# Kernel tuning notes

Measured on AMD Instinct MI355X. Metric: run time of the kernel, lower is better.

The kernel has to match this reference:

```python
import jax, jax.numpy as jnp
from jax import lax
import numpy as np

DECAY = 0.5   # LIF membrane leak factor
VTH = 1.0     # firing threshold


def _conv(x, w, stride, pad):
    # x: [B,C,H,W], w: [O,I,kh,kw]
    return lax.conv_general_dilated(
        x, w, (stride, stride), [(pad, pad), (pad, pad)],
        dimension_numbers=('NCHW', 'OIHW', 'NCHW'))


def _convT(x, w, b, stride=2, pad=1):
    # torch ConvTranspose2d(in,out,k,stride,pad): w is [Cin,Cout,k,k]
    k = w.shape[-1]
    wf = jnp.flip(w, (-2, -1)).transpose(1, 0, 2, 3)  # -> [Cout,Cin,k,k]
    y = lax.conv_general_dilated(
        x, wf, (1, 1), [(k - 1 - pad, k - 1 - pad)] * 2,
        lhs_dilation=(stride, stride),
        dimension_numbers=('NCHW', 'OIHW', 'NCHW'))
    return y + b[None, :, None, None]


def setup_inputs() -> dict:
    key = jax.random.key(0)
    ks = jax.random.split(key, 8)
    T, B = 16, 32
    x_seq = (jax.random.uniform(ks[0], (T, B, 1, 100, 368)) < 0.1).astype(jnp.float32)

    def p(k, shape, fan_in):
        return jax.random.normal(k, shape, jnp.float32) * (1.0 / np.sqrt(fan_in))

    return {
        'x_seq': x_seq,
        'w1': p(ks[1], (16, 1, 5, 5), 25),
        'w2': p(ks[2], (32, 16, 3, 3), 16 * 9),
        'wd': p(ks[3], (64, 32, 3, 3), 32 * 9),
        'bd': jnp.zeros((64,), jnp.float32),
        'wt1': p(ks[4], (64, 32, 4, 4), 64 * 16),
        'bt1': jnp.zeros((32,), jnp.float32),
        'wt2': p(ks[5], (32, 2, 4, 4), 32 * 16),
        'bt2': jnp.zeros((2,), jnp.float32),
        'actual_batch_size': 32,
    }


def reference(x_seq, w1, w2, wd, bd, wt1, bt1, wt2, bt2, actual_batch_size):
    B = x_seq.shape[1]
    dt = x_seq.dtype
    mem1 = jnp.zeros((B, 16, 50, 184), dt)
    mem2 = jnp.zeros((B, 32, 25, 92), dt)

    def step(carry, x):
        m1, m2 = carry
        # spiking conv layer 1: leaky integrate, fire, hard reset
        m1 = m1 * DECAY + _conv(x, w1, 2, 2)
        s1 = (m1 >= VTH).astype(dt)
        m1 = m1 * (1.0 - s1)
        # spiking conv layer 2 (return_dense -> membrane kept for decoder)
        m2 = m2 * DECAY + _conv(s1, w2, 2, 1)
        s2 = (m2 >= VTH).astype(dt)
        m2 = m2 * (1.0 - s2)
        return (m1, m2), None

    (mem1, mem2), _ = lax.scan(step, (mem1, mem2), x_seq)

    # dense CNN decoder on final membrane state
    h = jax.nn.relu(_conv(mem2, wd, 1, 1) + bd[None, :, None, None])   # [B,64,25,92]
    h = jax.nn.relu(_convT(h, wt1, bt1))                               # [B,32,50,184]
    out = jax.nn.softplus(_convT(h, wt2, bt2))                         # [B,2,100,368]
    inv_tau_c_pred = out[:, 0:1]
    alpha_pred = out[:, 1:2]
    return inv_tau_c_pred, alpha_pred
```

## Files before the change

### kernel.cpp

```cpp
#include <hip/hip_runtime.h>
#include <hip/hip_bf16.h>
#include <cstddef>


#define T_STEPS 16
#define NB 32
#define H0 100
#define W0 368
#define C1 16
#define H1 50
#define W1 184
#define C2 32
#define H2 25
#define W2 92
#define CD 64
#define WPR 6
#define SITES2 2300
#define SITES1 9200
#define NPOS1 (NB * H1 * W1)

using f32x16 = __attribute__((ext_vector_type(16))) float;
using f32x4  = __attribute__((ext_vector_type(4))) float;
using s16x8  = __attribute__((ext_vector_type(8))) short;

__device__ inline unsigned short f2bf(float f) {
    union { float f; unsigned int u; } v; v.f = f;
    unsigned int r = v.u + 0x7fffu + ((v.u >> 16) & 1u);
    return (unsigned short)(r >> 16);
}
__device__ inline float bf2f(unsigned short u) {
    union { unsigned int u; float f; } v; v.u = ((unsigned int)u) << 16;
    return v.f;
}
__device__ inline unsigned int pk2(float a, float b) {
    return (unsigned int)f2bf(a) | ((unsigned int)f2bf(b) << 16);
}
__device__ inline s16x8 ld8(const void* p) { return *reinterpret_cast<const s16x8*>(p); }

__global__ __launch_bounds__(256) void k_pack(const float* __restrict__ x,
                                              unsigned long long* __restrict__ xb) {
    int widx = blockIdx.x * 4 + (threadIdx.x >> 6);
    int lane = threadIdx.x & 63;
    int rowid = widx / WPR;
    int wcol  = widx - rowid * WPR;
    int col = (wcol << 6) + lane;
    const float* rp = x + (size_t)rowid * W0;
    float v = 0.f;
    if (col < W0) v = rp[col];
    unsigned long long m = __ballot(v != 0.f);
    if (lane == 0) xb[widx] = m;
}

__global__ __launch_bounds__(256) void k_mask(const unsigned long long* __restrict__ xb,
                                              unsigned int* __restrict__ bm) {
    int gid = blockIdx.x * blockDim.x + threadIdx.x;
    int t = gid / NPOS1;
    int site = gid - t * NPOS1;
    int x1 = site % W1;
    int tq = site / W1;
    int y1 = tq % H1;
    int b  = tq / H1;
    const int iy0 = 2 * y1 - 2;
    const int ix0 = 2 * x1 - 2;
    const int wi = ix0 >> 6;
    const int sh = ix0 & 63;
    const unsigned long long* xp = xb + ((size_t)(t * NB + b) * H0) * WPR;
    unsigned int bits25 = 0;
#pragma unroll
    for (int ky = 0; ky < 5; ++ky) {
        int iy = iy0 + ky;
        if (iy < 0 || iy >= H0) continue;
        const unsigned long long* row = xp + (size_t)iy * WPR;
        unsigned long long a = (wi >= 0) ? row[wi] : 0ull;
        unsigned long long bw = (wi + 1 < WPR) ? row[wi + 1] : 0ull;
        unsigned long long chunk = a >> sh;
        if (sh) chunk |= (bw << (64 - sh));
        bits25 |= ((unsigned int)chunk & 31u) << (5 * ky);
    }
    bm[gid] = bits25;
}

__global__ __launch_bounds__(256) void k_snn1(const unsigned int* __restrict__ bm,
                                              const unsigned short* __restrict__ w1b3,
                                              unsigned char* __restrict__ s1b) {
    __shared__ uint4 lut[256];
    {
        int m = (int)threadIdx.x;
        unsigned int wv[4];
#pragma unroll
        for (int h = 0; h < 4; ++h) {
            unsigned int lo = (m >> (2 * h)) & 1u, hb = (m >> (2 * h + 1)) & 1u;
            wv[h] = (lo ? 0x3F80u : 0u) | (hb ? 0x3F800000u : 0u);
        }
        lut[m] = make_uint4(wv[0], wv[1], wv[2], wv[3]);
    }
    __syncthreads();

    int wave = threadIdx.x >> 6;
    int lane = threadIdx.x & 63;
    int col = lane & 15;
    int hi  = lane >> 4;
    int base = (blockIdx.x * 4 + wave) * 64;

    s16x8 af0 = ld8((const char*)w1b3 + (size_t)((0 * 16 + col) * 32 + hi * 8) * 2);
    s16x8 af1 = ld8((const char*)w1b3 + (size_t)((1 * 16 + col) * 32 + hi * 8) * 2);
    s16x8 af2 = ld8((const char*)w1b3 + (size_t)((2 * 16 + col) * 32 + hi * 8) * 2);

    f32x4 acc0 = {}, acc1 = {}, acc2 = {}, acc3 = {};

    unsigned int cm0, cm1, cm2, cm3;
    {
        const unsigned int* bp = bm + base;
        cm0 = bp[col]; cm1 = bp[16 + col]; cm2 = bp[32 + col]; cm3 = bp[48 + col];
    }

    for (int t = 0; t < T_STEPS; ++t) {
        unsigned int nm0 = 0, nm1 = 0, nm2 = 0, nm3 = 0;
        if (t < T_STEPS - 1) {
            const unsigned int* bp = bm + (size_t)(t + 1) * NPOS1 + base;
            nm0 = bp[col]; nm1 = bp[16 + col]; nm2 = bp[32 + col]; nm3 = bp[48 + col];
        }
#pragma unroll
        for (int e = 0; e < 4; ++e) {
            acc0[e] *= 0.5f; acc1[e] *= 0.5f; acc2[e] *= 0.5f; acc3[e] *= 0.5f;
        }
#pragma unroll
        for (int g = 0; g < 4; ++g) {
            unsigned int sb = (g == 0) ? cm0 : (g == 1) ? cm1 : (g == 2) ? cm2 : cm3;
            unsigned int byte = (sb >> (hi * 8)) & 0xFFu;
            s16x8 bf = *reinterpret_cast<const s16x8*>(&lut[byte]);
            f32x4& ac = (g == 0) ? acc0 : (g == 1) ? acc1 : (g == 2) ? acc2 : acc3;
            ac = __builtin_amdgcn_mfma_f32_16x16x32_bf16(af0, bf, ac, 0, 0, 0);
            ac = __builtin_amdgcn_mfma_f32_16x16x32_bf16(af1, bf, ac, 0, 0, 0);
            ac = __builtin_amdgcn_mfma_f32_16x16x32_bf16(af2, bf, ac, 0, 0, 0);
        }
#pragma unroll
        for (int g = 0; g < 4; ++g) {
            f32x4& ac = (g == 0) ? acc0 : (g == 1) ? acc1 : (g == 2) ? acc2 : acc3;
            unsigned int nib = 0;
#pragma unroll
            for (int e = 0; e < 4; ++e) {
                float v = ac[e];
                bool s = (v >= 1.0f);
                if (s) nib |= (1u << e);
                ac[e] = s ? 0.f : v;
            }
            unsigned int mk = nib << ((hi & 1) * 4);
            mk |= __shfl_xor(mk, 16, 64);
            if (hi == 0)
                s1b[(size_t)(t * 2 + 0) * NPOS1 + base + g * 16 + col] = (unsigned char)mk;
            else if (hi == 2)
                s1b[(size_t)(t * 2 + 1) * NPOS1 + base + g * 16 + col] = (unsigned char)mk;
        }
        cm0 = nm0; cm1 = nm1; cm2 = nm2; cm3 = nm3;
    }
}

__global__ __launch_bounds__(256) void k_snn2(const unsigned char* __restrict__ s1b,
                                              const unsigned short* __restrict__ w2b3,
                                              unsigned short* __restrict__ mem2bf) {
    __shared__ uint4 lut[256];
    {
        int m = (int)threadIdx.x;
        unsigned int wv[4];
#pragma unroll
        for (int h = 0; h < 4; ++h) {
            unsigned int lo = (m >> (2 * h)) & 1u, hb = (m >> (2 * h + 1)) & 1u;
            wv[h] = (lo ? 0x3F80u : 0u) | (hb ? 0x3F800000u : 0u);
        }
        lut[m] = make_uint4(wv[0], wv[1], wv[2], wv[3]);
    }
    __syncthreads();

    int wave = threadIdx.x >> 6;
    int lane = threadIdx.x & 63;
    int col = lane & 31, hi = lane >> 5;
    int gsite = (blockIdx.x * 4 + wave) * 32 + col;
    int b = gsite / SITES2;
    int rest = gsite % SITES2;
    int y2 = rest / W2, x2 = rest % W2;

    int toff[9]; bool tval[9];
#pragma unroll
    for (int ky = 0; ky < 3; ++ky)
#pragma unroll
        for (int kx = 0; kx < 3; ++kx) {
            int iy = 2 * y2 + ky - 1, ix = 2 * x2 + kx - 1;
            tval[ky * 3 + kx] = iy >= 0 && iy < H1 && ix >= 0 && ix < W1;
            toff[ky * 3 + kx] = iy * W1 + ix;
        }

    const char* ab = (const char*)w2b3;
    s16x8 a0[9], a1[9], a2[9];
#pragma unroll
    for (int s = 0; s < 9; ++s) {
        int ko = (s * 16 + hi * 8) * 2;
        a0[s] = ld8(ab + (col * 144) * 2 + ko);
        a1[s] = ld8(ab + ((32 + col) * 144) * 2 + ko);
        a2[s] = ld8(ab + ((64 + col) * 144) * 2 + ko);
    }

    f32x16 acc = {};

    unsigned int msk[9];
    {
        const unsigned char* spk = s1b + (size_t)hi * NPOS1 + (size_t)b * (H1 * W1);
#pragma unroll
        for (int i = 0; i < 9; ++i)
            msk[i] = tval[i] ? (unsigned int)spk[toff[i]] : 0u;
    }

    for (int t = 0; t < T_STEPS; ++t) {
        unsigned int nmsk[9];
#pragma unroll
        for (int i = 0; i < 9; ++i) nmsk[i] = 0u;
        if (t < T_STEPS - 1) {
            const unsigned char* spk = s1b + (size_t)((t + 1) * 2 + hi) * NPOS1 + (size_t)b * (H1 * W1);
#pragma unroll
            for (int i = 0; i < 9; ++i)
                nmsk[i] = tval[i] ? (unsigned int)spk[toff[i]] : 0u;
        }

#pragma unroll
        for (int e = 0; e < 16; ++e) acc[e] *= 0.5f;

#pragma unroll
        for (int s = 0; s < 9; ++s) {
            s16x8 bf = *reinterpret_cast<const s16x8*>(&lut[msk[s]]);
            acc = __builtin_amdgcn_mfma_f32_32x32x16_bf16(a0[s], bf, acc, 0, 0, 0);
            acc = __builtin_amdgcn_mfma_f32_32x32x16_bf16(a1[s], bf, acc, 0, 0, 0);
            acc = __builtin_amdgcn_mfma_f32_32x32x16_bf16(a2[s], bf, acc, 0, 0, 0);
        }
#pragma unroll
        for (int e = 0; e < 16; ++e) {
            float v = acc[e];
            acc[e] = (v >= 1.0f) ? 0.f : v;
        }
#pragma unroll
        for (int i = 0; i < 9; ++i) msk[i] = nmsk[i];
    }

    char* obase = (char*)(mem2bf + (size_t)gsite * C2);
#pragma unroll
    for (int q = 0; q < 4; ++q) {
        int co = 8 * q + 4 * hi;
        uint2 u;
        u.x = pk2(acc[4 * q + 0], acc[4 * q + 1]);
        u.y = pk2(acc[4 * q + 2], acc[4 * q + 3]);
        *(uint2*)(obase + co * 2) = u;
    }
}

__global__ __launch_bounds__(256) void k_repackb(const float* __restrict__ wd,
                                                 const float* __restrict__ wt1,
                                                 const float* __restrict__ wt2,
                                                 const float* __restrict__ w2,
                                                 const float* __restrict__ w1,
                                                 unsigned short* __restrict__ wdb,
                                                 unsigned short* __restrict__ wt1b,
                                                 float* __restrict__ wt2k,
                                                 unsigned short* __restrict__ w2b3,
                                                 unsigned short* __restrict__ w1b3) {
    int gid = blockIdx.x * blockDim.x + threadIdx.x;
    if (gid < 64 * 288) {
        int co = gid / 288, k = gid % 288;
        int tap = k >> 5, ci = k & 31;
        wdb[gid] = f2bf(wd[((size_t)co * C2 + ci) * 9 + tap]);
    } else if (gid < 64 * 288 + 4 * 32 * 256) {
        int j = gid - 64 * 288;
        int par = j >> 13, co = (j >> 8) & 31, k = j & 255;
        int tap = k >> 6, ci = k & 63;
        int ty = tap >> 1, tx = tap & 1;
        int ry = par >> 1, rx = par & 1;
        int ky = ry ? (ty ? 0 : 2) : (ty ? 3 : 1);
        int kx = rx ? (tx ? 0 : 2) : (tx ? 3 : 1);
        wt1b[j] = f2bf(wt1[(((size_t)ci * 32 + co) * 4 + ky) * 4 + kx]);
    } else if (gid < 64 * 288 + 4 * 32 * 256 + 1024) {
        int j = gid - (64 * 288 + 4 * 32 * 256);
        int par = j >> 8, tap = (j >> 6) & 3, ci = (j >> 1) & 31, co = j & 1;
        int ty = tap >> 1, tx = tap & 1;
        int ry = par >> 1, rx = par & 1;
        int ky = ry ? (ty ? 0 : 2) : (ty ? 3 : 1);
        int kx = rx ? (tx ? 0 : 2) : (tx ? 3 : 1);
        wt2k[j] = wt2[(((size_t)ci * 2 + co) * 4 + ky) * 4 + kx];
    } else if (gid < 64 * 288 + 4 * 32 * 256 + 1024 + 3 * 32 * 144) {
        int j = gid - (64 * 288 + 4 * 32 * 256 + 1024);
        int p = j / 4608, rem = j % 4608;
        int co = rem / 144, k = rem % 144;
        int tap = k / 16, ci = k % 16;
        float w = w2[((size_t)co * C1 + ci) * 9 + tap];
        unsigned short b0 = f2bf(w);
        float r1 = w - bf2f(b0);
        unsigned short b1 = f2bf(r1);
        float r2 = r1 - bf2f(b1);
        unsigned short b2 = f2bf(r2);
        w2b3[j] = (p == 0) ? b0 : (p == 1) ? b1 : b2;
    } else if (gid < 64 * 288 + 4 * 32 * 256 + 1024 + 3 * 32 * 144 + 3 * 16 * 32) {
        int j = gid - (64 * 288 + 4 * 32 * 256 + 1024 + 3 * 32 * 144);
        int p = j / 512, rem = j % 512;
        int co = rem / 32, k = rem % 32;
        float w = (k < 25) ? w1[co * 25 + k] : 0.f;
        unsigned short b0 = f2bf(w);
        float r1 = w - bf2f(b0);
        unsigned short b1 = f2bf(r1);
        float r2 = r1 - bf2f(b1);
        unsigned short b2 = f2bf(r2);
        w1b3[j] = (p == 0) ? b0 : (p == 1) ? b1 : b2;
    }
}

__global__ __launch_bounds__(256) void k_convd(const unsigned short* __restrict__ mem2bf,
                                               const unsigned short* __restrict__ wdb,
                                               const float* __restrict__ bd,
                                               unsigned short* __restrict__ h1bf) {
    int wave = threadIdx.x >> 6;
    int lane = threadIdx.x & 63;
    int col = lane & 31, hi = lane >> 5;
    int cog = blockIdx.y;
    int b = blockIdx.z;
    int n0 = (blockIdx.x * 4 + wave) * 32;
    int site = n0 + col;
    bool sval = site < SITES2;
    int sc = sval ? site : 0;
    int yy = sc / W2, xx = sc % W2;

    const char* ibase = (const char*)(mem2bf + (size_t)b * SITES2 * C2);
    int toff[9];
    bool tval[9];
#pragma unroll
    for (int ky = 0; ky < 3; ++ky)
#pragma unroll
        for (int kx = 0; kx < 3; ++kx) {
            int iy = yy + ky - 1, ix = xx + kx - 1;
            bool v = sval && iy >= 0 && iy < H2 && ix >= 0 && ix < W2;
            tval[ky * 3 + kx] = v;
            toff[ky * 3 + kx] = (iy * W2 + ix) * (C2 * 2);
        }

    const s16x8 zero = {0, 0, 0, 0, 0, 0, 0, 0};
    s16x8 bfr[18];
#pragma unroll
    for (int s = 0; s < 18; ++s) {
        int tap = s >> 1;
        int boff = (s & 1) * 32 + hi * 16;
        bfr[s] = tval[tap] ? ld8(ibase + toff[tap] + boff) : zero;
    }
    const char* abase = (const char*)wdb + (size_t)(cog * 32 + col) * 576 + hi * 16;
    s16x8 ar[18];
#pragma unroll
    for (int s = 0; s < 18; ++s)
        ar[s] = ld8(abase + s * 32);

    f32x16 acc = {};
#pragma unroll
    for (int s = 0; s < 18; ++s)
        acc = __builtin_amdgcn_mfma_f32_32x32x16_bf16(ar[s], bfr[s], acc, 0, 0, 0);

    if (!sval) return;
    char* obase = (char*)(h1bf + ((size_t)b * SITES2 + site) * CD);
#pragma unroll
    for (int q = 0; q < 4; ++q) {
        int co = cog * 32 + 8 * q + 4 * hi;
        float v0 = fmaxf(acc[4 * q + 0] + bd[co + 0], 0.f);
        float v1 = fmaxf(acc[4 * q + 1] + bd[co + 1], 0.f);
        float v2 = fmaxf(acc[4 * q + 2] + bd[co + 2], 0.f);
        float v3 = fmaxf(acc[4 * q + 3] + bd[co + 3], 0.f);
        uint2 u; u.x = pk2(v0, v1); u.y = pk2(v2, v3);
        *(uint2*)(obase + co * 2) = u;
    }
}

__global__ __launch_bounds__(256) void k_convt1(const unsigned short* __restrict__ h1bf,
                                                const unsigned short* __restrict__ wt1b,
                                                const float* __restrict__ bt1,
                                                unsigned short* __restrict__ h2bf) {
    int par = threadIdx.x >> 6;
    int lane = threadIdx.x & 63;
    int col = lane & 31, hi = lane >> 5;
    int ry = par >> 1, rx = par & 1;
    int b = blockIdx.z;
    int bx = blockIdx.x;
    int tile = (bx & 7) * 9 + (bx >> 3);
    int n0 = tile * 32;

    const char* ibase = (const char*)(h1bf + (size_t)b * SITES2 * CD);
    int site = n0 + col;
    bool sv = site < SITES2;
    int sc = sv ? site : 0;
    int m = sc / W2, n = sc % W2;
    int iy1 = m + (ry ? 1 : -1);
    int ix1 = n + (rx ? 1 : -1);
    bool y1v = iy1 >= 0 && iy1 < H2;
    bool x1v = ix1 >= 0 && ix1 < W2;
    int toff[4]; bool tval[4];
#pragma unroll
    for (int t = 0; t < 4; ++t) {
        int ty = t >> 1, tx = t & 1;
        int iy = ty ? iy1 : m;
        int ix = tx ? ix1 : n;
        tval[t] = sv && (ty ? y1v : true) && (tx ? x1v : true);
        toff[t] = (iy * W2 + ix) * (CD * 2);
    }

    const s16x8 zero = {0, 0, 0, 0, 0, 0, 0, 0};
    s16x8 bfr[16];
#pragma unroll
    for (int s = 0; s < 16; ++s) {
        int tap = s >> 2;
        int boff = (s & 3) * 32 + hi * 16;
        bfr[s] = tval[tap] ? ld8(ibase + toff[tap] + boff) : zero;
    }
    const char* abase = (const char*)(wt1b + (size_t)par * 32 * 256) + (size_t)col * 512 + hi * 16;
    s16x8 ar[16];
#pragma unroll
    for (int s = 0; s < 16; ++s)
        ar[s] = ld8(abase + s * 32);

    f32x16 acc = {};
#pragma unroll
    for (int s = 0; s < 16; ++s)
        acc = __builtin_amdgcn_mfma_f32_32x32x16_bf16(ar[s], bfr[s], acc, 0, 0, 0);

    if (!sv) return;
    int oy = 2 * m + ry, ox = 2 * n + rx;
    char* obase = (char*)(h2bf + ((size_t)b * SITES1 + (size_t)oy * W1 + ox) * C2);
#pragma unroll
    for (int q = 0; q < 4; ++q) {
        int co = 8 * q + 4 * hi;
        float v0 = fmaxf(acc[4 * q + 0] + bt1[co + 0], 0.f);
        float v1 = fmaxf(acc[4 * q + 1] + bt1[co + 1], 0.f);
        float v2 = fmaxf(acc[4 * q + 2] + bt1[co + 2], 0.f);
        float v3 = fmaxf(acc[4 * q + 3] + bt1[co + 3], 0.f);
        uint2 u; u.x = pk2(v0, v1); u.y = pk2(v2, v3);
        *(uint2*)(obase + co * 2) = u;
    }
}

__global__ __launch_bounds__(256) void k_convt2(const unsigned short* __restrict__ h2bf,
                                                const float* __restrict__ wt2k,
                                                const float* __restrict__ bt2,
                                                float* __restrict__ out) {
    int i = blockIdx.x * blockDim.x + threadIdx.x;
    if (i >= SITES1) return;
    int par = blockIdx.y;
    int ry = par >> 1, rx = par & 1;
    int b = blockIdx.z;
    int m = i / W1, n = i % W1;
    int iy1 = m + (ry ? 1 : -1);
    int ix1 = n + (rx ? 1 : -1);
    bool y1v = iy1 >= 0 && iy1 < H1;
    bool x1v = ix1 >= 0 && ix1 < W1;

    float a0 = bt2[0], a1 = bt2[1];
    const unsigned short* ib = h2bf + (size_t)b * SITES1 * C2;
#pragma unroll
    for (int t = 0; t < 4; ++t) {
        int ty = t >> 1, tx = t & 1;
        if ((ty && !y1v) || (tx && !x1v)) continue;
        int iy = ty ? iy1 : m;
        int ix = tx ? ix1 : n;
        const unsigned short* p = ib + ((size_t)iy * W1 + ix) * C2;
        const float* w = wt2k + ((size_t)par * 4 + t) * 64;
#pragma unroll
        for (int g = 0; g < 4; ++g) {
            s16x8 v8 = ld8(p + g * 8);
#pragma unroll
            for (int e = 0; e < 8; ++e) {
                float v = bf2f((unsigned short)v8[e]);
                int ci = g * 8 + e;
                a0 += v * w[2 * ci];
                a1 += v * w[2 * ci + 1];
            }
        }
    }
    int oy = 2 * m + ry, ox = 2 * n + rx;
    size_t base_o = (size_t)b * (H0 * W0) + (size_t)oy * W0 + ox;
    out[base_o] = fmaxf(a0, 0.f) + log1pf(expf(-fabsf(a0)));
    out[(size_t)NB * H0 * W0 + base_o] = fmaxf(a1, 0.f) + log1pf(expf(-fabsf(a1)));
}

extern "C" void kernel_launch(void* const* d_in, const int* in_sizes, int n_in,
                              void* d_out, int out_size, void* d_ws, size_t ws_size,
                              hipStream_t stream) {
    const float* x   = (const float*)d_in[0];
    const float* w1  = (const float*)d_in[1];
    const float* w2  = (const float*)d_in[2];
    const float* wd  = (const float*)d_in[3];
    const float* bd  = (const float*)d_in[4];
    const float* wt1 = (const float*)d_in[5];
    const float* bt1 = (const float*)d_in[6];
    const float* wt2 = (const float*)d_in[7];
    const float* bt2 = (const float*)d_in[8];
    float* out = (float*)d_out;

    char* ws = (char*)d_ws;
    unsigned char* s1b     = (unsigned char*)(ws);
    unsigned short* mem2bf = (unsigned short*)(ws + 9420800);
    unsigned short* h1bf   = (unsigned short*)(ws + 14131200);
    unsigned short* h2bf   = (unsigned short*)(ws + 23552000);
    unsigned long long* xb = (unsigned long long*)(ws + 42393600);
    unsigned short* wdb    = (unsigned short*)(ws + 44851200);
    unsigned short* wt1b   = (unsigned short*)(ws + 44888064);
    float* wt2k            = (float*)(ws + 44953600);
    unsigned short* w2b3   = (unsigned short*)(ws + 44957696);
    unsigned short* w1b3   = (unsigned short*)(ws + 44985344);
    unsigned int* bm       = (unsigned int*)(ws + 44988416);

    {
        int n = 64 * 288 + 4 * 32 * 256 + 1024 + 3 * 32 * 144 + 3 * 16 * 32;
        k_repackb<<<(n + 255) / 256, 256, 0, stream>>>(wd, wt1, wt2, w2, w1,
                                                       wdb, wt1b, wt2k, w2b3, w1b3);
    }
    {
        k_pack<<<76800, 256, 0, stream>>>(x, xb);
    }
    {
        k_mask<<<18400, 256, 0, stream>>>(xb, bm);
    }
    {
        k_snn1<<<1150, 256, 0, stream>>>(bm, w1b3, s1b);
    }
    {
        k_snn2<<<575, 256, 0, stream>>>(s1b, w2b3, mem2bf);
    }
    {
        dim3 g(18, 2, NB);
        k_convd<<<g, 256, 0, stream>>>(mem2bf, wdb, bd, h1bf);
    }
    {
        dim3 g(72, 1, NB);
        k_convt1<<<g, 256, 0, stream>>>(h1bf, wt1b, bt1, h2bf);
    }
    {
        dim3 g(36, 4, NB);
        k_convt2<<<g, 256, 0, stream>>>(h2bf, wt2k, bt2, out);
    }
}
```

Baseline: 208.6 us.

## Parallelize SNN layer-2 across timesteps with per-wave conv and LDS recurrence

```diff
diff --git a/kernel.cpp b/kernel.cpp
--- a/kernel.cpp
+++ b/kernel.cpp
@@ -156,11 +156,12 @@
     }
 }
 
-__global__ __launch_bounds__(256) void k_snn2(const unsigned char* __restrict__ s1b,
-                                              const unsigned short* __restrict__ w2b3,
-                                              unsigned short* __restrict__ mem2bf) {
+__global__ __launch_bounds__(512, 4) void k_snn2(const unsigned char* __restrict__ s1b,
+                                                 const unsigned short* __restrict__ w2b3,
+                                                 unsigned short* __restrict__ mem2bf) {
     __shared__ uint4 lut[256];
-    {
+    __shared__ float ct[8][1088];
+    if (threadIdx.x < 256) {
         int m = (int)threadIdx.x;
         unsigned int wv[4];
 #pragma unroll
@@ -175,7 +176,7 @@
     int wave = threadIdx.x >> 6;
     int lane = threadIdx.x & 63;
     int col = lane & 31, hi = lane >> 5;
-    int gsite = (blockIdx.x * 4 + wave) * 32 + col;
+    int gsite = blockIdx.x * 32 + col;
     int b = gsite / SITES2;
     int rest = gsite % SITES2;
     int y2 = rest / W2, x2 = rest % W2;
@@ -190,65 +191,59 @@
             toff[ky * 3 + kx] = iy * W1 + ix;
         }
 
+    unsigned int mskA[9], mskB[9];
+    {
+        const unsigned char* spkA = s1b + (size_t)(wave * 2 + hi) * NPOS1 + (size_t)b * (H1 * W1);
+        const unsigned char* spkB = s1b + (size_t)((wave + 8) * 2 + hi) * NPOS1 + (size_t)b * (H1 * W1);
+#pragma unroll
+        for (int i = 0; i < 9; ++i) {
+            mskA[i] = tval[i] ? (unsigned int)spkA[toff[i]] : 0u;
+            mskB[i] = tval[i] ? (unsigned int)spkB[toff[i]] : 0u;
+        }
+    }
+
     const char* ab = (const char*)w2b3;
-    s16x8 a0[9], a1[9], a2[9];
-#pragma unroll
-    for (int s = 0; s < 9; ++s) {
-        int ko = (s * 16 + hi * 8) * 2;
-        a0[s] = ld8(ab + (col * 144) * 2 + ko);
-        a1[s] = ld8(ab + ((32 + col) * 144) * 2 + ko);
-        a2[s] = ld8(ab + ((64 + col) * 144) * 2 + ko);
-    }
-
-    f32x16 acc = {};
-
-    unsigned int msk[9];
-    {
-        const unsigned char* spk = s1b + (size_t)hi * NPOS1 + (size_t)b * (H1 * W1);
-#pragma unroll
-        for (int i = 0; i < 9; ++i)
-            msk[i] = tval[i] ? (unsigned int)spk[toff[i]] : 0u;
-    }
-
-    for (int t = 0; t < T_STEPS; ++t) {
-        unsigned int nmsk[9];
-#pragma unroll
-        for (int i = 0; i < 9; ++i) nmsk[i] = 0u;
-        if (t < T_STEPS - 1) {
-            const unsigned char* spk = s1b + (size_t)((t + 1) * 2 + hi) * NPOS1 + (size_t)b * (H1 * W1);
-#pragma unroll
-            for (int i = 0; i < 9; ++i)
-                nmsk[i] = tval[i] ? (unsigned int)spk[toff[i]] : 0u;
-        }
-
-#pragma unroll
-        for (int e = 0; e < 16; ++e) acc[e] *= 0.5f;
-
+    const int koBase = hi * 16;
+
+    int co = threadIdx.x & 31;
+    int sA = threadIdx.x >> 5;
+    int e2 = (co & 3) | ((co >> 3) << 2);
+    int hi2 = (co >> 2) & 1;
+    int lA = hi2 * 32 + sA;
+    int lB = lA + 16;
+    float mA = 0.f, mB = 0.f;
+
+#pragma unroll
+    for (int p = 0; p < 2; ++p) {
+        f32x16 acc = {};
 #pragma unroll
         for (int s = 0; s < 9; ++s) {
-            s16x8 bf = *reinterpret_cast<const s16x8*>(&lut[msk[s]]);
-            acc = __builtin_amdgcn_mfma_f32_32x32x16_bf16(a0[s], bf, acc, 0, 0, 0);
-            acc = __builtin_amdgcn_mfma_f32_32x32x16_bf16(a1[s], bf, acc, 0, 0, 0);
-            acc = __builtin_amdgcn_mfma_f32_32x32x16_bf16(a2[s], bf, acc, 0, 0, 0);
-        }
-#pragma unroll
-        for (int e = 0; e < 16; ++e) {
-            float v = acc[e];
-            acc[e] = (v >= 1.0f) ? 0.f : v;
-        }
-#pragma unroll
-        for (int i = 0; i < 9; ++i) msk[i] = nmsk[i];
-    }
-
-    char* obase = (char*)(mem2bf + (size_t)gsite * C2);
-#pragma unroll
-    for (int q = 0; q < 4; ++q) {
-        int co = 8 * q + 4 * hi;
-        uint2 u;
-        u.x = pk2(acc[4 * q + 0], acc[4 * q + 1]);
-        u.y = pk2(acc[4 * q + 2], acc[4 * q + 3]);
-        *(uint2*)(obase + co * 2) = u;
-    }
+            unsigned int byte = p ? mskB[s] : mskA[s];
+            s16x8 bf = *reinterpret_cast<const s16x8*>(&lut[byte]);
+            s16x8 a0 = ld8(ab + (col * 144) * 2 + s * 32 + koBase);
+            s16x8 a1 = ld8(ab + ((32 + col) * 144) * 2 + s * 32 + koBase);
+            s16x8 a2 = ld8(ab + ((64 + col) * 144) * 2 + s * 32 + koBase);
+            acc = __builtin_amdgcn_mfma_f32_32x32x16_bf16(a0, bf, acc, 0, 0, 0);
+            acc = __builtin_amdgcn_mfma_f32_32x32x16_bf16(a1, bf, acc, 0, 0, 0);
+            acc = __builtin_amdgcn_mfma_f32_32x32x16_bf16(a2, bf, acc, 0, 0, 0);
+        }
+        float* dst = &ct[wave][lane * 17];
+#pragma unroll
+        for (int e = 0; e < 16; ++e) dst[e] = acc[e];
+        __syncthreads();
+#pragma unroll
+        for (int k = 0; k < 8; ++k) {
+            float cA = ct[k][lA * 17 + e2];
+            float cB = ct[k][lB * 17 + e2];
+            mA = mA * 0.5f + cA; mA = (mA >= 1.0f) ? 0.f : mA;
+            mB = mB * 0.5f + cB; mB = (mB >= 1.0f) ? 0.f : mB;
+        }
+        __syncthreads();
+    }
+
+    size_t obase = (size_t)blockIdx.x * 32;
+    mem2bf[(obase + sA) * C2 + co]      = f2bf(mA);
+    mem2bf[(obase + sA + 16) * C2 + co] = f2bf(mB);
 }
 
 __global__ __launch_bounds__(256) void k_repackb(const float* __restrict__ wd,
@@ -521,7 +516,7 @@
         k_snn1<<<1150, 256, 0, stream>>>(bm, w1b3, s1b);
     }
     {
-        k_snn2<<<575, 256, 0, stream>>>(s1b, w2b3, mem2bf);
+        k_snn2<<<2300, 512, 0, stream>>>(s1b, w2b3, mem2bf);
     }
     {
         dim3 g(18, 2, NB);
```

Result: slower. 237.6 us (+13.9%).
